# Performance work log

Hardware: AMD Instinct MI355X
Metric: run time of the kernel (lower is better)

The kernel has to match this reference:

```python
import jax, jax.numpy as jnp
import numpy as np

EPS = 1e-9


def setup_inputs() -> dict:
    key = jax.random.key(0)
    k1, k2 = jax.random.split(key)
    B, IN, OUT = 16384, 2048, 2048
    x = jax.random.normal(k1, (B, IN), dtype=jnp.float32)
    w = jax.random.normal(k2, (OUT, IN), dtype=jnp.float32)
    # set_weight_norms_to(initial_weight_norm=0.01): rescale each row's L2 norm to 0.01
    wn = jnp.linalg.norm(w, axis=1, keepdims=True)
    weight = 0.01 * w / (wn + 1e-10)
    logprior = jnp.zeros((OUT,), dtype=jnp.float32)
    lamb = jnp.float32(4.0)  # initial_lambda
    return {"x": x, "weight": weight, "logprior": logprior, "lamb": lamb}


def reference(x, weight, logprior, lamb):
    # L2-normalize inputs per row
    x_n = x / (jnp.linalg.norm(x, axis=1, keepdims=True) + EPS)  # [B, IN]
    # L2-normalize weight rows -> cosine similarities
    W = weight / (jnp.linalg.norm(weight, axis=1, keepdims=True) + EPS)  # [OUT, IN]
    a = x_n @ W.T  # [B, OUT] cosine sims
    # RePU inhibition, triangle=False -> setpoint 0
    u = jax.nn.relu(a)
    un = u / (jnp.max(u) + EPS)  # global max normalization
    # power-law with logprior; safe power (0**lamb == 0) to keep grads clean
    pos = un > 0
    ulamb = jnp.where(pos, jnp.where(pos, un, 1.0) ** lamb, 0.0) * jnp.exp(logprior)
    y = ulamb / (jnp.sum(ulamb, axis=1, keepdims=True) + EPS)
    return y
```

## Files before the change

### kernel.cpp

```cpp
#include <hip/hip_runtime.h>
#include <hip/hip_bf16.h>

typedef unsigned short u16;
typedef __attribute__((ext_vector_type(8))) short bf16x8;
typedef __attribute__((ext_vector_type(4))) float f32x4;

#define EPSN 1e-9f


__device__ __forceinline__ u16 f2bf(float f) {
    union { float f; unsigned int u; } c; c.f = f;
    unsigned int u = c.u;
    unsigned int r = (u + 0x7FFFu + ((u >> 16) & 1u)) >> 16;
    return (u16)r;
}

__device__ __forceinline__ void load16_to_lds(const void* g, void* l) {
    __builtin_amdgcn_global_load_lds(
        (const __attribute__((address_space(1))) void*)g,
        (__attribute__((address_space(3))) void*)l,
        16, 0, 0);
}

#define MAXQ 8
__global__ __launch_bounds__(256) void normalize_cast(
    const float* __restrict__ X, u16* __restrict__ Y, int ncols) {
    const size_t row = blockIdx.x;
    const float4* xr = (const float4*)(X + row * (size_t)ncols);
    const int nq = ncols >> 2;

    float4 v[MAXQ];
    float ss = 0.f;
    #pragma unroll
    for (int k = 0; k < MAXQ; ++k) {
        int i = threadIdx.x + k * 256;
        if (i < nq) {
            v[k] = xr[i];
            ss += v[k].x*v[k].x + v[k].y*v[k].y + v[k].z*v[k].z + v[k].w*v[k].w;
        }
    }
    #pragma unroll
    for (int o = 32; o > 0; o >>= 1) ss += __shfl_down(ss, o);

    __shared__ float red[4];
    __shared__ float scale_sh;
    const int lane = threadIdx.x & 63, wv = threadIdx.x >> 6;
    if (lane == 0) red[wv] = ss;
    __syncthreads();
    if (threadIdx.x == 0) {
        float t = red[0] + red[1] + red[2] + red[3];
        scale_sh = 1.f / (sqrtf(t) + EPSN);
    }
    __syncthreads();
    const float s = scale_sh;

    ushort4* yr = (ushort4*)(Y + row * (size_t)ncols);
    #pragma unroll
    for (int k = 0; k < MAXQ; ++k) {
        int i = threadIdx.x + k * 256;
        if (i < nq) {
            ushort4 o4;
            o4.x = f2bf(v[k].x * s); o4.y = f2bf(v[k].y * s);
            o4.z = f2bf(v[k].z * s); o4.w = f2bf(v[k].w * s);
            yr[i] = o4;
        }
    }
}

__global__ void prep_explp(const float* __restrict__ lp, float* __restrict__ out, int n) {
    int i = blockIdx.x * blockDim.x + threadIdx.x;
    if (i < n) out[i] = expf(lp[i]);
}

#define BK 64

__global__ __launch_bounds__(256, 2) void gemm_softhebb(
    const u16* __restrict__ A, const u16* __restrict__ B,
    const float* __restrict__ explp, const float* __restrict__ lambp,
    float* __restrict__ Ul, float* __restrict__ rowsum,
    int M, int N, int K) {
    __shared__ __align__(16) u16 lA[128 * BK];
    __shared__ __align__(16) u16 lB[128 * BK];

    const int tid  = threadIdx.x;
    const int lane = tid & 63;
    const int wm   = (tid >> 6) & 1;
    const int wn   = tid >> 7;
    const int row0 = blockIdx.y * 128;
    const int col0 = blockIdx.x * 128;

    f32x4 acc[4][4] = {};

    const u16* ap[4];
    const u16* bp[4];
    #pragma unroll
    for (int p = 0; p < 4; ++p) {
        int c = p * 256 + tid;
        int r = c >> 3;
        int o = ((c & 7) ^ (r & 7)) * 8;
        ap[p] = A + (size_t)(row0 + r) * K + o;
        bp[p] = B + (size_t)(col0 + r) * K + o;
    }

    for (int k0 = 0; k0 < K; k0 += BK) {
        #pragma unroll
        for (int p = 0; p < 4; ++p) {
            int c = p * 256 + tid;
            load16_to_lds(ap[p] + k0, &lA[c * 8]);
            load16_to_lds(bp[p] + k0, &lB[c * 8]);
        }
        __syncthreads();

        #pragma unroll
        for (int s = 0; s < 2; ++s) {
            const int pos = (((s << 2) + (lane >> 4)) ^ (lane & 7)) * 8;
            bf16x8 af[4], bfr[4];
            #pragma unroll
            for (int i = 0; i < 4; ++i) {
                int r = wm * 64 + i * 16 + (lane & 15);
                af[i] = *(const bf16x8*)&lA[r * 64 + pos];
            }
            #pragma unroll
            for (int j = 0; j < 4; ++j) {
                int r = wn * 64 + j * 16 + (lane & 15);
                bfr[j] = *(const bf16x8*)&lB[r * 64 + pos];
            }
            #pragma unroll
            for (int i = 0; i < 4; ++i)
                #pragma unroll
                for (int j = 0; j < 4; ++j)
                    acc[i][j] = __builtin_amdgcn_mfma_f32_16x16x32_bf16(
                        af[i], bfr[j], acc[i][j], 0, 0, 0);
        }
        __syncthreads();
    }

    const float lam = *lambp;
    const bool lam4 = (lam == 4.0f);
    float el[4];
    #pragma unroll
    for (int j = 0; j < 4; ++j)
        el[j] = explp[col0 + wn * 64 + j * 16 + (lane & 15)];

    #pragma unroll
    for (int i = 0; i < 4; ++i) {
        #pragma unroll
        for (int p = 0; p < 4; ++p) {
            const int m = row0 + wm * 64 + i * 16 + (lane >> 4) * 4 + p;
            float* outrow = Ul + (size_t)m * N + col0 + wn * 64 + (lane & 15);
            float rs = 0.f;
            #pragma unroll
            for (int j = 0; j < 4; ++j) {
                float a = acc[i][j][p];
                float u = 0.f;
                if (a > 0.f) {
                    float pw;
                    if (lam4) { float a2 = a * a; pw = a2 * a2; }
                    else      { pw = __powf(a, lam); }
                    u = pw * el[j];
                }
                outrow[j * 16] = u;
                rs += u;
            }
            rs += __shfl_xor(rs, 1);
            rs += __shfl_xor(rs, 2);
            rs += __shfl_xor(rs, 4);
            rs += __shfl_xor(rs, 8);
            if ((lane & 15) == 0) atomicAdd(&rowsum[m], rs);
        }
    }
}

__global__ __launch_bounds__(256) void finalize_row(
    float* __restrict__ Ul, const float* __restrict__ rowsum, int nq) {
    const size_t row = blockIdx.x;
    const float inv = 1.f / (rowsum[row] + EPSN);
    float4* p = (float4*)(Ul + row * (size_t)nq * 4);
    for (int i = threadIdx.x; i < nq; i += 256) {
        float4 v = p[i];
        v.x *= inv; v.y *= inv; v.z *= inv; v.w *= inv;
        p[i] = v;
    }
}

static inline size_t align256(size_t x) { return (x + 255) & ~(size_t)255; }

extern "C" void kernel_launch(void* const* d_in, const int* in_sizes, int n_in,
                              void* d_out, int out_size, void* d_ws, size_t ws_size,
                              hipStream_t stream) {
    const float* x        = (const float*)d_in[0];
    const float* w        = (const float*)d_in[1];
    const float* logprior = (const float*)d_in[2];
    const float* lamb     = (const float*)d_in[3];
    const int OUT = in_sizes[2];
    const int IN  = in_sizes[1] / OUT;
    const int B   = in_sizes[0] / IN;
    float* out = (float*)d_out;

    char* ws = (char*)d_ws;
    size_t off = 0;
    u16* xn = (u16*)(ws + off);        off += align256((size_t)B * IN * sizeof(u16));
    u16* wn = (u16*)(ws + off);        off += align256((size_t)OUT * IN * sizeof(u16));
    float* rowsum = (float*)(ws + off); off += align256((size_t)B * sizeof(float));
    float* explp  = (float*)(ws + off); off += align256((size_t)OUT * sizeof(float));

    hipMemsetAsync(rowsum, 0, (size_t)B * sizeof(float), stream);
    normalize_cast<<<B, 256, 0, stream>>>(x, xn, IN);
    normalize_cast<<<OUT, 256, 0, stream>>>(w, wn, IN);
    prep_explp<<<(OUT + 255) / 256, 256, 0, stream>>>(logprior, explp, OUT);

    dim3 grid(OUT / 128, B / 128);
    gemm_softhebb<<<grid, 256, 0, stream>>>(xn, wn, explp, lamb, out, rowsum, B, OUT, IN);

    finalize_row<<<B, 256, 0, stream>>>(out, rowsum, OUT / 4);
}
```

Baseline: 414.5 us.

## Store unnormalized activations as bf16 intermediate and fuse prep kernels

```diff
diff --git a/kernel.cpp b/kernel.cpp
--- a/kernel.cpp
+++ b/kernel.cpp
@@ -3,6 +3,7 @@
 
 typedef unsigned short u16;
 typedef __attribute__((ext_vector_type(8))) short bf16x8;
+typedef __attribute__((ext_vector_type(8))) unsigned short u16x8;
 typedef __attribute__((ext_vector_type(4))) float f32x4;
 
 #define EPSN 1e-9f
@@ -15,6 +16,11 @@
     return (u16)r;
 }
 
+__device__ __forceinline__ float bf2f(u16 b) {
+    union { unsigned int u; float f; } c; c.u = ((unsigned int)b) << 16;
+    return c.f;
+}
+
 __device__ __forceinline__ void load16_to_lds(const void* g, void* l) {
     __builtin_amdgcn_global_load_lds(
         (const __attribute__((address_space(1))) void*)g,
@@ -22,42 +28,35 @@
         16, 0, 0);
 }
 
-#define MAXQ 8
-__global__ __launch_bounds__(256) void normalize_cast(
-    const float* __restrict__ X, u16* __restrict__ Y, int ncols) {
-    const size_t row = blockIdx.x;
-    const float4* xr = (const float4*)(X + row * (size_t)ncols);
+__global__ __launch_bounds__(256) void normalize_cast_rows(
+    const float* __restrict__ X, u16* __restrict__ Y,
+    float* __restrict__ rowzero, int ncols, int nrows) {
+    const int row  = blockIdx.x * 4 + (threadIdx.x >> 6);
+    if (row >= nrows) return;
+    const int lane = threadIdx.x & 63;
+    const float4* xr = (const float4*)(X + (size_t)row * ncols);
     const int nq = ncols >> 2;
 
-    float4 v[MAXQ];
+    float4 v[8];
     float ss = 0.f;
     #pragma unroll
-    for (int k = 0; k < MAXQ; ++k) {
-        int i = threadIdx.x + k * 256;
+    for (int k = 0; k < 8; ++k) {
+        int i = lane + (k << 6);
         if (i < nq) {
             v[k] = xr[i];
             ss += v[k].x*v[k].x + v[k].y*v[k].y + v[k].z*v[k].z + v[k].w*v[k].w;
         }
     }
     #pragma unroll
-    for (int o = 32; o > 0; o >>= 1) ss += __shfl_down(ss, o);
-
-    __shared__ float red[4];
-    __shared__ float scale_sh;
-    const int lane = threadIdx.x & 63, wv = threadIdx.x >> 6;
-    if (lane == 0) red[wv] = ss;
-    __syncthreads();
-    if (threadIdx.x == 0) {
-        float t = red[0] + red[1] + red[2] + red[3];
-        scale_sh = 1.f / (sqrtf(t) + EPSN);
-    }
-    __syncthreads();
-    const float s = scale_sh;
-
-    ushort4* yr = (ushort4*)(Y + row * (size_t)ncols);
-    #pragma unroll
-    for (int k = 0; k < MAXQ; ++k) {
-        int i = threadIdx.x + k * 256;
+    for (int o = 32; o > 0; o >>= 1) ss += __shfl_xor(ss, o);
+    const float s = 1.f / (sqrtf(ss) + EPSN);
+
+    if (rowzero && lane == 0) rowzero[row] = 0.f;
+
+    ushort4* yr = (ushort4*)(Y + (size_t)row * ncols);
+    #pragma unroll
+    for (int k = 0; k < 8; ++k) {
+        int i = lane + (k << 6);
         if (i < nq) {
             ushort4 o4;
             o4.x = f2bf(v[k].x * s); o4.y = f2bf(v[k].y * s);
@@ -67,17 +66,13 @@
     }
 }
 
-__global__ void prep_explp(const float* __restrict__ lp, float* __restrict__ out, int n) {
-    int i = blockIdx.x * blockDim.x + threadIdx.x;
-    if (i < n) out[i] = expf(lp[i]);
-}
-
 #define BK 64
 
+template <bool BF16OUT>
 __global__ __launch_bounds__(256, 2) void gemm_softhebb(
     const u16* __restrict__ A, const u16* __restrict__ B,
-    const float* __restrict__ explp, const float* __restrict__ lambp,
-    float* __restrict__ Ul, float* __restrict__ rowsum,
+    const float* __restrict__ logprior, const float* __restrict__ lambp,
+    void* __restrict__ Uout, float* __restrict__ rowsum,
     int M, int N, int K) {
     __shared__ __align__(16) u16 lA[128 * BK];
     __shared__ __align__(16) u16 lB[128 * BK];
@@ -140,14 +135,14 @@
     float el[4];
     #pragma unroll
     for (int j = 0; j < 4; ++j)
-        el[j] = explp[col0 + wn * 64 + j * 16 + (lane & 15)];
+        el[j] = expf(logprior[col0 + wn * 64 + j * 16 + (lane & 15)]);
 
     #pragma unroll
     for (int i = 0; i < 4; ++i) {
         #pragma unroll
         for (int p = 0; p < 4; ++p) {
             const int m = row0 + wm * 64 + i * 16 + (lane >> 4) * 4 + p;
-            float* outrow = Ul + (size_t)m * N + col0 + wn * 64 + (lane & 15);
+            const size_t base = (size_t)m * N + col0 + wn * 64 + (lane & 15);
             float rs = 0.f;
             #pragma unroll
             for (int j = 0; j < 4; ++j) {
@@ -159,8 +154,14 @@
                     else      { pw = __powf(a, lam); }
                     u = pw * el[j];
                 }
-                outrow[j * 16] = u;
-                rs += u;
+                if (BF16OUT) {
+                    u16 r = f2bf(u);
+                    ((u16*)Uout)[base + j * 16] = r;
+                    rs += bf2f(r);
+                } else {
+                    ((float*)Uout)[base + j * 16] = u;
+                    rs += u;
+                }
             }
             rs += __shfl_xor(rs, 1);
             rs += __shfl_xor(rs, 2);
@@ -171,7 +172,28 @@
     }
 }
 
-__global__ __launch_bounds__(256) void finalize_row(
+__global__ __launch_bounds__(256) void finalize_rows_bf16(
+    const u16* __restrict__ U, const float* __restrict__ rowsum,
+    float* __restrict__ Y, int ncols) {
+    const int row  = blockIdx.x * 4 + (threadIdx.x >> 6);
+    const int lane = threadIdx.x & 63;
+    const float inv = 1.f / (rowsum[row] + EPSN);
+    const u16x8* ur = (const u16x8*)(U + (size_t)row * ncols);
+    float* yr = Y + (size_t)row * ncols;
+    const int n8 = ncols >> 3;
+    for (int i = lane; i < n8; i += 64) {
+        u16x8 u8 = ur[i];
+        f32x4 lo, hi;
+        lo[0] = bf2f(u8[0]) * inv; lo[1] = bf2f(u8[1]) * inv;
+        lo[2] = bf2f(u8[2]) * inv; lo[3] = bf2f(u8[3]) * inv;
+        hi[0] = bf2f(u8[4]) * inv; hi[1] = bf2f(u8[5]) * inv;
+        hi[2] = bf2f(u8[6]) * inv; hi[3] = bf2f(u8[7]) * inv;
+        __builtin_nontemporal_store(lo, (f32x4*)(yr + i * 8));
+        __builtin_nontemporal_store(hi, (f32x4*)(yr + i * 8 + 4));
+    }
+}
+
+__global__ __launch_bounds__(256) void finalize_row_f32(
     float* __restrict__ Ul, const float* __restrict__ rowsum, int nq) {
     const size_t row = blockIdx.x;
     const float inv = 1.f / (rowsum[row] + EPSN);
@@ -199,18 +221,23 @@
 
     char* ws = (char*)d_ws;
     size_t off = 0;
-    u16* xn = (u16*)(ws + off);        off += align256((size_t)B * IN * sizeof(u16));
-    u16* wn = (u16*)(ws + off);        off += align256((size_t)OUT * IN * sizeof(u16));
+    u16* xn = (u16*)(ws + off);         off += align256((size_t)B * IN * sizeof(u16));
+    u16* wn = (u16*)(ws + off);         off += align256((size_t)OUT * IN * sizeof(u16));
     float* rowsum = (float*)(ws + off); off += align256((size_t)B * sizeof(float));
-    float* explp  = (float*)(ws + off); off += align256((size_t)OUT * sizeof(float));
-
-    hipMemsetAsync(rowsum, 0, (size_t)B * sizeof(float), stream);
-    normalize_cast<<<B, 256, 0, stream>>>(x, xn, IN);
-    normalize_cast<<<OUT, 256, 0, stream>>>(w, wn, IN);
-    prep_explp<<<(OUT + 255) / 256, 256, 0, stream>>>(logprior, explp, OUT);
+    u16* ub = (u16*)(ws + off);         off += align256((size_t)B * OUT * sizeof(u16));
+    const bool bf16path = (off <= ws_size);
+
+    normalize_cast_rows<<<(B + 3) / 4, 256, 0, stream>>>(x, xn, rowsum, IN, B);
+    normalize_cast_rows<<<(OUT + 3) / 4, 256, 0, stream>>>(w, wn, nullptr, IN, OUT);
 
     dim3 grid(OUT / 128, B / 128);
-    gemm_softhebb<<<grid, 256, 0, stream>>>(xn, wn, explp, lamb, out, rowsum, B, OUT, IN);
-
-    finalize_row<<<B, 256, 0, stream>>>(out, rowsum, OUT / 4);
-}
+    if (bf16path) {
+        gemm_softhebb<true><<<grid, 256, 0, stream>>>(
+            xn, wn, logprior, lamb, (void*)ub, rowsum, B, OUT, IN);
+        finalize_rows_bf16<<<B / 4, 256, 0, stream>>>(ub, rowsum, out, OUT);
+    } else {
+        gemm_softhebb<false><<<grid, 256, 0, stream>>>(
+            xn, wn, logprior, lamb, (void*)out, rowsum, B, OUT, IN);
+        finalize_row_f32<<<B, 256, 0, stream>>>(out, rowsum, OUT / 4);
+    }
+}
```

Result: slower. 426.5 us (+2.9%).
